# Kernel tuning notes

Measured on AMD Instinct MI355X. Metric: run time of the kernel, lower is better.

Reference implementation:

```python
import jax, jax.numpy as jnp
import numpy as np
from jax import lax

K = 8  # diffusion channels
T = 3  # diffusion steps


def setup_inputs() -> dict:
    key = jax.random.key(0)
    k1, k2, k3 = jax.random.split(key, 3)
    x = jax.random.normal(k1, (16, 1, 512, 512), dtype=jnp.float32)
    # per-step conv weights [T, out=k, in=1, kh, kw] and biases [T, k]
    W = jax.random.normal(k2, (T, K, 1, 3, 3), dtype=jnp.float32) * 0.1
    b = jax.random.normal(k3, (T, K), dtype=jnp.float32) * 0.1
    return {"x": x, "W": W, "b": b}


def _g(d):
    # mode 1 edge-stopping function: exp(-|d| / (1 + d^2))
    return jnp.exp(-jnp.abs(d) / (1.0 + d * d))


def reference(x, W, b):
    in_x = x  # [N,1,H,W]
    for t in range(T):
        d1 = lax.conv_general_dilated(
            in_x, W[t], window_strides=(1, 1), padding="SAME",
            dimension_numbers=("NCHW", "OIHW", "NCHW"),
        ) + b[t][None, :, None, None]  # [N,K,H,W]
        features = _g(d1) * d1
        # squash_tensor: sum over the K channels, keep channel dim of 1
        in_x = in_x - jnp.sum(features, axis=1, keepdims=True) / K
    return in_x
```

## Files before the change

### kernel.cpp

```cpp
#include <hip/hip_runtime.h>

static constexpr int IMG = 512;

__device__ __forceinline__ float gd_acc(float d, float acc) {
    const float t    = fmaf(d, d, 1.0f);
    const float rinv = __builtin_amdgcn_rcpf(t);
    const float e    = __builtin_amdgcn_exp2f(
                           -1.442695040888963f * __builtin_fabsf(d) * rinv);
    return fmaf(e, d, acc);
}

__global__ __launch_bounds__(256) void ad_step(
    const float* __restrict__ in, float* __restrict__ outp,
    const float* __restrict__ Wt, const float* __restrict__ bt)
{
    const int tid = threadIdx.x;
    const int x0  = blockIdx.x * 64 + (tid & 15) * 4;
    const int y   = blockIdx.y * 16 + (tid >> 4);
    const float* __restrict__ src = in + (size_t)blockIdx.z * (IMG * IMG);

    float L[3][12];
    const bool xfast = (x0 >= 4) && (x0 <= 504);
#pragma unroll
    for (int dy = 0; dy < 3; ++dy) {
        const int yy = y + dy - 1;
        const bool rowok = (unsigned)yy < (unsigned)IMG;
        if (xfast && rowok) {
            const float* p = src + yy * IMG + x0 - 4;
            *(float4*)&L[dy][0] = *(const float4*)(p);
            *(float4*)&L[dy][4] = *(const float4*)(p + 4);
            *(float4*)&L[dy][8] = *(const float4*)(p + 8);
        } else {
#pragma unroll
            for (int j = 0; j < 12; ++j) {
                const int col = x0 - 4 + j;
                L[dy][j] = (rowok && (unsigned)col < (unsigned)IMG)
                               ? src[yy * IMG + col] : 0.f;
            }
        }
    }

    float acc[4] = {0.f, 0.f, 0.f, 0.f};
#pragma unroll
    for (int k = 0; k < 8; ++k) {
        const float w0 = Wt[9*k+0], w1 = Wt[9*k+1], w2 = Wt[9*k+2];
        const float w3 = Wt[9*k+3], w4 = Wt[9*k+4], w5 = Wt[9*k+5];
        const float w6 = Wt[9*k+6], w7 = Wt[9*k+7], w8 = Wt[9*k+8];
        const float bk = bt[k];
#pragma unroll
        for (int i = 0; i < 4; ++i) {
            float d = bk;
            d = fmaf(w0, L[0][i+3], d);
            d = fmaf(w1, L[0][i+4], d);
            d = fmaf(w2, L[0][i+5], d);
            d = fmaf(w3, L[1][i+3], d);
            d = fmaf(w4, L[1][i+4], d);
            d = fmaf(w5, L[1][i+5], d);
            d = fmaf(w6, L[2][i+3], d);
            d = fmaf(w7, L[2][i+4], d);
            d = fmaf(w8, L[2][i+5], d);
            acc[i] = gd_acc(d, acc[i]);
        }
    }

    float4 v;
    v.x = L[1][4] - acc[0] * 0.125f;
    v.y = L[1][5] - acc[1] * 0.125f;
    v.z = L[1][6] - acc[2] * 0.125f;
    v.w = L[1][7] - acc[3] * 0.125f;
    *(float4*)&outp[(size_t)blockIdx.z * (IMG * IMG) + y * IMG + x0] = v;
}

static constexpr int TXF = 64;
static constexpr int TYF = 16;
static constexpr int LST = 72;
static constexpr int SROWS  = TYF + 6;
static constexpr int NSTAGE = SROWS * 18;

template<int WOFF, int NR, int RLO, int NG, bool TO_GLOBAL>
__device__ __forceinline__ void diffuse_step(
    const float* __restrict__ prev, float* __restrict__ cur,
    const float* __restrict__ Wt, const float* __restrict__ bt,
    int xoff, int ty0, int tx0, int tid, float* __restrict__ gout)
{
    constexpr int LOADW  = WOFF ? 8 : 6;
    constexpr int NITEMS = NR * NG;

    float L0[LOADW], L1[LOADW], L2[LOADW];
    {
        const int idx0 = (tid < NITEMS) ? tid : 0;
        const int rr = idx0 / NG, j = idx0 - rr * NG;
        const float* base = prev + (RLO + rr - 1) * LST + 4 * j;
        *(float4*)&L0[0] = *(const float4*)(base);
        *(float4*)&L1[0] = *(const float4*)(base + LST);
        *(float4*)&L2[0] = *(const float4*)(base + 2 * LST);
        if (WOFF) {
            *(float4*)&L0[4] = *(const float4*)(base + 4);
            *(float4*)&L1[4] = *(const float4*)(base + LST + 4);
            *(float4*)&L2[4] = *(const float4*)(base + 2 * LST + 4);
        } else {
            *(float2*)&L0[4] = *(const float2*)(base + 4);
            *(float2*)&L1[4] = *(const float2*)(base + LST + 4);
            *(float2*)&L2[4] = *(const float2*)(base + 2 * LST + 4);
        }
    }

    for (int idx = tid; idx < NITEMS; idx += 64) {
        float P0[LOADW], P1[LOADW], P2[LOADW];
        {
            const int nidx = (idx + 64 < NITEMS) ? (idx + 64) : idx;
            const int rr = nidx / NG, j = nidx - rr * NG;
            const float* base = prev + (RLO + rr - 1) * LST + 4 * j;
            *(float4*)&P0[0] = *(const float4*)(base);
            *(float4*)&P1[0] = *(const float4*)(base + LST);
            *(float4*)&P2[0] = *(const float4*)(base + 2 * LST);
            if (WOFF) {
                *(float4*)&P0[4] = *(const float4*)(base + 4);
                *(float4*)&P1[4] = *(const float4*)(base + LST + 4);
                *(float4*)&P2[4] = *(const float4*)(base + 2 * LST + 4);
            } else {
                *(float2*)&P0[4] = *(const float2*)(base + 4);
                *(float2*)&P1[4] = *(const float2*)(base + LST + 4);
                *(float2*)&P2[4] = *(const float2*)(base + 2 * LST + 4);
            }
        }

        const int rr = idx / NG, j = idx - rr * NG;
        const int r  = RLO + rr, c0 = 4 * j;

        float acc[4] = {0.f, 0.f, 0.f, 0.f};
#pragma unroll
        for (int k = 0; k < 8; ++k) {
            const float w0 = Wt[9*k+0], w1 = Wt[9*k+1], w2 = Wt[9*k+2];
            const float w3 = Wt[9*k+3], w4 = Wt[9*k+4], w5 = Wt[9*k+5];
            const float w6 = Wt[9*k+6], w7 = Wt[9*k+7], w8 = Wt[9*k+8];
            const float bk = bt[k];
#pragma unroll
            for (int i = 0; i < 4; ++i) {
                float d = bk;
                d = fmaf(w0, L0[WOFF+i],   d);
                d = fmaf(w1, L0[WOFF+i+1], d);
                d = fmaf(w2, L0[WOFF+i+2], d);
                d = fmaf(w3, L1[WOFF+i],   d);
                d = fmaf(w4, L1[WOFF+i+1], d);
                d = fmaf(w5, L1[WOFF+i+2], d);
                d = fmaf(w6, L2[WOFF+i],   d);
                d = fmaf(w7, L2[WOFF+i+1], d);
                d = fmaf(w8, L2[WOFF+i+2], d);
                acc[i] = gd_acc(d, acc[i]);
            }
        }

        float4 v;
        v.x = L1[WOFF+1] - acc[0] * 0.125f;
        v.y = L1[WOFF+2] - acc[1] * 0.125f;
        v.z = L1[WOFF+3] - acc[2] * 0.125f;
        v.w = L1[WOFF+4] - acc[3] * 0.125f;

        const int gy = ty0 - 3 + r;
        if (TO_GLOBAL) {
            *(float4*)&gout[gy * IMG + tx0 + c0] = v;
        } else {
            const bool ry  = (unsigned)gy < (unsigned)IMG;
            const int  gx0 = xoff + c0;
            v.x = (ry && (unsigned)(gx0 + 0) < (unsigned)IMG) ? v.x : 0.f;
            v.y = (ry && (unsigned)(gx0 + 1) < (unsigned)IMG) ? v.y : 0.f;
            v.z = (ry && (unsigned)(gx0 + 2) < (unsigned)IMG) ? v.z : 0.f;
            v.w = (ry && (unsigned)(gx0 + 3) < (unsigned)IMG) ? v.w : 0.f;
            *(float4*)&cur[r * LST + c0] = v;
        }

#pragma unroll
        for (int q = 0; q < LOADW; ++q) { L0[q] = P0[q]; L1[q] = P1[q]; L2[q] = P2[q]; }
    }
}

__global__ __launch_bounds__(64) void deep_ad_fused(
    const float* __restrict__ x, const float* __restrict__ W,
    const float* __restrict__ b, float* __restrict__ out)
{
    __shared__ float A[SROWS * LST];
    __shared__ float Bs[SROWS * LST];

    const int tid = threadIdx.x;
    const int tx0 = blockIdx.x * TXF;
    const int ty0 = blockIdx.y * TYF;
    const float* xin  = x   + (size_t)blockIdx.z * (IMG * IMG);
    float*       gout = out + (size_t)blockIdx.z * (IMG * IMG);

    {
        float4 sv[7];
#pragma unroll
        for (int q = 0; q < 7; ++q) {
            const int item = tid + 64 * q;
            const int rr = item / 18, j = item - rr * 18;
            const int gy = ty0 - 3 + rr;
            const int gx = tx0 - 4 + 4 * j;
            float4 v = {0.f, 0.f, 0.f, 0.f};
            if (item < NSTAGE && (unsigned)gy < (unsigned)IMG && (unsigned)gx < (unsigned)IMG)
                v = *(const float4*)(xin + gy * IMG + gx);
            sv[q] = v;
        }
#pragma unroll
        for (int q = 0; q < 7; ++q) {
            const int item = tid + 64 * q;
            if (item < NSTAGE) *(float4*)&A[item * 4] = sv[q];
        }
    }
    __syncthreads();

    diffuse_step<1, TYF + 4, 1, 17, false>(A,  Bs, W + 0,   b + 0,  tx0 - 2, ty0, tx0, tid, nullptr);
    __syncthreads();
    diffuse_step<0, TYF + 2, 2, 17, false>(Bs, A,  W + 72,  b + 8,  tx0 - 1, ty0, tx0, tid, nullptr);
    __syncthreads();
    diffuse_step<0, TYF,     3, 16, true >(A, nullptr, W + 144, b + 16, 0, ty0, tx0, tid, gout);
}

extern "C" void kernel_launch(void* const* d_in, const int* in_sizes, int n_in,
                              void* d_out, int out_size, void* d_ws, size_t ws_size,
                              hipStream_t stream)
{
    const float* x = (const float*)d_in[0];
    const float* W = (const float*)d_in[1];
    const float* b = (const float*)d_in[2];
    float* out = (float*)d_out;
    const int N = in_sizes[0] / (IMG * IMG);

    const size_t imgBytes = (size_t)N * IMG * IMG * sizeof(float);
    if (ws_size >= imgBytes) {
        float* ws = (float*)d_ws;
        dim3 g(IMG / 64, IMG / 16, N);
        ad_step<<<g, 256, 0, stream>>>(x,   out, W + 0,   b + 0);
        ad_step<<<g, 256, 0, stream>>>(out, ws,  W + 72,  b + 8);
        ad_step<<<g, 256, 0, stream>>>(ws,  out, W + 144, b + 16);
    } else {
        dim3 grid(IMG / TXF, IMG / TYF, N);
        deep_ad_fused<<<grid, 64, 0, stream>>>(x, W, b, out);
    }
}
```

Measured before the change: 115.3 us.

## Use packed fp16 dot2 for conv taps with pre-packed weights

Adds a small kernel that packs each step's 3x3 weights into fp16 pairs plus fp32 tap and bias in workspace. The three-step path converts input neighbourhoods to packed half2 and computes eight of the nine taps with v_dot2 instructions, cutting the FMA count per channel. This lowers precision of the convolution inputs and weights to fp16 (round-toward-zero), which risks accuracy, and adds an extra launch. The fused fallback also drops its software prefetch of the next item's rows.

```diff
diff --git a/kernel.cpp b/kernel.cpp
--- a/kernel.cpp
+++ b/kernel.cpp
@@ -1,4 +1,6 @@
 #include <hip/hip_runtime.h>
+
+typedef __fp16 half2_t __attribute__((ext_vector_type(2)));
 
 static constexpr int IMG = 512;
 
@@ -10,9 +12,26 @@
     return fmaf(e, d, acc);
 }
 
+__global__ void pack_weights(const float* __restrict__ W,
+                             const float* __restrict__ b,
+                             float* __restrict__ wp)
+{
+    const int id = threadIdx.x;
+    if (id >= 24) return;
+    const int t = id / 8, k = id % 8;
+    const float* w = W + (t * 8 + k) * 9;
+    float* o = wp + t * 64 + k * 8;
+    o[0] = __builtin_bit_cast(float, __builtin_amdgcn_cvt_pkrtz(w[0], w[1]));
+    o[1] = __builtin_bit_cast(float, __builtin_amdgcn_cvt_pkrtz(w[2], w[3]));
+    o[2] = __builtin_bit_cast(float, __builtin_amdgcn_cvt_pkrtz(w[4], w[5]));
+    o[3] = __builtin_bit_cast(float, __builtin_amdgcn_cvt_pkrtz(w[6], w[7]));
+    o[4] = w[8];
+    o[5] = b[t * 8 + k];
+}
+
 __global__ __launch_bounds__(256) void ad_step(
     const float* __restrict__ in, float* __restrict__ outp,
-    const float* __restrict__ Wt, const float* __restrict__ bt)
+    const float* __restrict__ wp)
 {
     const int tid = threadIdx.x;
     const int x0  = blockIdx.x * 64 + (tid & 15) * 4;
@@ -40,25 +59,31 @@
         }
     }
 
+    half2_t PA[4], PB[4], PC[4], PD[4];
+#pragma unroll
+    for (int i = 0; i < 4; ++i) {
+        PA[i] = __builtin_amdgcn_cvt_pkrtz(L[0][3+i], L[0][4+i]);
+        PB[i] = __builtin_amdgcn_cvt_pkrtz(L[0][5+i], L[1][3+i]);
+        PC[i] = __builtin_amdgcn_cvt_pkrtz(L[1][4+i], L[1][5+i]);
+        PD[i] = __builtin_amdgcn_cvt_pkrtz(L[2][3+i], L[2][4+i]);
+    }
+
     float acc[4] = {0.f, 0.f, 0.f, 0.f};
 #pragma unroll
     for (int k = 0; k < 8; ++k) {
-        const float w0 = Wt[9*k+0], w1 = Wt[9*k+1], w2 = Wt[9*k+2];
-        const float w3 = Wt[9*k+3], w4 = Wt[9*k+4], w5 = Wt[9*k+5];
-        const float w6 = Wt[9*k+6], w7 = Wt[9*k+7], w8 = Wt[9*k+8];
-        const float bk = bt[k];
+        const float* wk = wp + k * 8;
+        const half2_t wA = __builtin_bit_cast(half2_t, wk[0]);
+        const half2_t wB = __builtin_bit_cast(half2_t, wk[1]);
+        const half2_t wC = __builtin_bit_cast(half2_t, wk[2]);
+        const half2_t wD = __builtin_bit_cast(half2_t, wk[3]);
+        const float   w8 = wk[4], bk = wk[5];
 #pragma unroll
         for (int i = 0; i < 4; ++i) {
-            float d = bk;
-            d = fmaf(w0, L[0][i+3], d);
-            d = fmaf(w1, L[0][i+4], d);
-            d = fmaf(w2, L[0][i+5], d);
-            d = fmaf(w3, L[1][i+3], d);
-            d = fmaf(w4, L[1][i+4], d);
-            d = fmaf(w5, L[1][i+5], d);
-            d = fmaf(w6, L[2][i+3], d);
-            d = fmaf(w7, L[2][i+4], d);
-            d = fmaf(w8, L[2][i+5], d);
+            float d = fmaf(w8, L[2][5+i], bk);
+            d = __builtin_amdgcn_fdot2(wA, PA[i], d, false);
+            d = __builtin_amdgcn_fdot2(wB, PB[i], d, false);
+            d = __builtin_amdgcn_fdot2(wC, PC[i], d, false);
+            d = __builtin_amdgcn_fdot2(wD, PD[i], d, false);
             acc[i] = gd_acc(d, acc[i]);
         }
     }
@@ -86,11 +111,12 @@
     constexpr int LOADW  = WOFF ? 8 : 6;
     constexpr int NITEMS = NR * NG;
 
-    float L0[LOADW], L1[LOADW], L2[LOADW];
-    {
-        const int idx0 = (tid < NITEMS) ? tid : 0;
-        const int rr = idx0 / NG, j = idx0 - rr * NG;
-        const float* base = prev + (RLO + rr - 1) * LST + 4 * j;
+    for (int idx = tid; idx < NITEMS; idx += 64) {
+        const int rr = idx / NG, j = idx - rr * NG;
+        const int r  = RLO + rr, c0 = 4 * j;
+        const float* base = prev + (r - 1) * LST + c0;
+
+        float L0[LOADW], L1[LOADW], L2[LOADW];
         *(float4*)&L0[0] = *(const float4*)(base);
         *(float4*)&L1[0] = *(const float4*)(base + LST);
         *(float4*)&L2[0] = *(const float4*)(base + 2 * LST);
@@ -103,30 +129,6 @@
             *(float2*)&L1[4] = *(const float2*)(base + LST + 4);
             *(float2*)&L2[4] = *(const float2*)(base + 2 * LST + 4);
         }
-    }
-
-    for (int idx = tid; idx < NITEMS; idx += 64) {
-        float P0[LOADW], P1[LOADW], P2[LOADW];
-        {
-            const int nidx = (idx + 64 < NITEMS) ? (idx + 64) : idx;
-            const int rr = nidx / NG, j = nidx - rr * NG;
-            const float* base = prev + (RLO + rr - 1) * LST + 4 * j;
-            *(float4*)&P0[0] = *(const float4*)(base);
-            *(float4*)&P1[0] = *(const float4*)(base + LST);
-            *(float4*)&P2[0] = *(const float4*)(base + 2 * LST);
-            if (WOFF) {
-                *(float4*)&P0[4] = *(const float4*)(base + 4);
-                *(float4*)&P1[4] = *(const float4*)(base + LST + 4);
-                *(float4*)&P2[4] = *(const float4*)(base + 2 * LST + 4);
-            } else {
-                *(float2*)&P0[4] = *(const float2*)(base + 4);
-                *(float2*)&P1[4] = *(const float2*)(base + LST + 4);
-                *(float2*)&P2[4] = *(const float2*)(base + 2 * LST + 4);
-            }
-        }
-
-        const int rr = idx / NG, j = idx - rr * NG;
-        const int r  = RLO + rr, c0 = 4 * j;
 
         float acc[4] = {0.f, 0.f, 0.f, 0.f};
 #pragma unroll
@@ -169,9 +171,6 @@
             v.w = (ry && (unsigned)(gx0 + 3) < (unsigned)IMG) ? v.w : 0.f;
             *(float4*)&cur[r * LST + c0] = v;
         }
-
-#pragma unroll
-        for (int q = 0; q < LOADW; ++q) { L0[q] = P0[q]; L1[q] = P1[q]; L2[q] = P2[q]; }
     }
 }
 
@@ -227,12 +226,15 @@
     const int N = in_sizes[0] / (IMG * IMG);
 
     const size_t imgBytes = (size_t)N * IMG * IMG * sizeof(float);
-    if (ws_size >= imgBytes) {
-        float* ws = (float*)d_ws;
+    const size_t wsNeed   = 32768 + imgBytes;
+    if (ws_size >= wsNeed) {
+        float* wp  = (float*)d_ws;
+        float* img = (float*)((char*)d_ws + 32768);
+        pack_weights<<<1, 64, 0, stream>>>(W, b, wp);
         dim3 g(IMG / 64, IMG / 16, N);
-        ad_step<<<g, 256, 0, stream>>>(x,   out, W + 0,   b + 0);
-        ad_step<<<g, 256, 0, stream>>>(out, ws,  W + 72,  b + 8);
-        ad_step<<<g, 256, 0, stream>>>(ws,  out, W + 144, b + 16);
+        ad_step<<<g, 256, 0, stream>>>(x,   out, wp + 0);
+        ad_step<<<g, 256, 0, stream>>>(out, img, wp + 64);
+        ad_step<<<g, 256, 0, stream>>>(img, out, wp + 128);
     } else {
         dim3 grid(IMG / TXF, IMG / TYF, N);
         deep_ad_fused<<<grid, 64, 0, stream>>>(x, W, b, out);
```

After: 120.6 us. +4.6%, slower.
